# Kernel optimization log

Hardware: AMD Instinct MI355X
Metric: run time of the kernel (lower is better)

The kernel has to match this reference:

```python
import jax, jax.numpy as jnp
import numpy as np

B, S, H, E, K = 8, 4096, 1024, 256, 64
NEG = -1e30  # finite stand-in for -inf to keep grads NaN-free


def setup_inputs() -> dict:
    key = jax.random.key(0)
    ks = jax.random.split(key, 8)
    Hq = H // 4
    sc = 0.02
    return {
        "hidden_states": jax.random.normal(ks[0], (B, S, H), dtype=jnp.float32),
        "attention_mask": jnp.ones((B, S), dtype=jnp.int32),
        "block_boundaries": jnp.sort(jax.random.randint(ks[1], (B, K), 0, S), axis=-1),
        "tok_w1": jax.random.normal(ks[2], (H, Hq), dtype=jnp.float32) * sc,
        "tok_b1": jnp.zeros((Hq,), dtype=jnp.float32),
        "tok_w2": jax.random.normal(ks[3], (Hq, 1), dtype=jnp.float32) * sc,
        "tok_b2": jnp.zeros((1,), dtype=jnp.float32),
        "blk_w1": jax.random.normal(ks[4], (H, Hq), dtype=jnp.float32) * sc,
        "blk_b1": jnp.zeros((Hq,), dtype=jnp.float32),
        "blk_w2": jax.random.normal(ks[5], (Hq, 1), dtype=jnp.float32) * sc,
        "blk_b2": jnp.zeros((1,), dtype=jnp.float32),
        "out_w": jax.random.normal(ks[6], (H, E), dtype=jnp.float32) * sc,
        "out_b": jnp.zeros((E,), dtype=jnp.float32),
    }


def _attn_scores(x, w1, b1, w2, b2):
    # Linear -> Tanh -> Linear(.,1), squeeze last dim
    return (jnp.tanh(x @ w1 + b1) @ w2 + b2)[..., 0]


def reference(hidden_states, attention_mask, block_boundaries,
              tok_w1, tok_b1, tok_w2, tok_b2,
              blk_w1, blk_b1, blk_w2, blk_b2,
              out_w, out_b):
    Bz, Sz, Hz = hidden_states.shape
    Kz = block_boundaries.shape[1]
    pos = jnp.arange(Sz)
    # token -> block id: last boundary <= pos (tokens before first boundary get -1)
    block_id = jax.vmap(lambda bnd: jnp.searchsorted(bnd, pos, side='right') - 1)(block_boundaries)  # [B,S]
    member = block_id[:, :, None] == jnp.arange(Kz)[None, None, :]      # [B,S,K]
    valid = (attention_mask == 1) & (block_id >= 0)                     # [B,S]
    m_full = member & valid[:, :, None]                                 # [B,S,K]

    # stage 1: per-block masked softmax over tokens
    tok_scores = _attn_scores(hidden_states, tok_w1, tok_b1, tok_w2, tok_b2)  # [B,S]
    s = jnp.where(m_full, tok_scores[:, :, None], NEG)
    mx = jnp.max(s, axis=1, keepdims=True)                              # [B,1,K]
    e = jnp.where(m_full, jnp.exp(tok_scores[:, :, None] - mx), 0.0)
    denom = jnp.sum(e, axis=1, keepdims=True)                           # [B,1,K]
    w = jnp.where(denom > 0, e / jnp.maximum(denom, 1e-30), 0.0)
    block_embed = jnp.einsum('bsk,bsd->bkd', w, hidden_states)          # [B,K,H]
    block_valid = denom[:, 0, :] > 0                                    # [B,K] (empty blocks dropped)

    # stage 2: softmax over (non-empty) blocks
    blk_scores = _attn_scores(block_embed, blk_w1, blk_b1, blk_w2, blk_b2)    # [B,K]
    blk_scores = jnp.where(block_valid, blk_scores, NEG)
    bw = jax.nn.softmax(blk_scores, axis=-1)
    func = jnp.einsum('bk,bkd->bd', bw, block_embed)                    # [B,H]

    out = func @ out_w + out_b                                          # [B,E]
    return out / jnp.maximum(jnp.linalg.norm(out, axis=-1, keepdims=True), 1e-12)
```

## Files before the change

kernel.cpp:

```cpp
#include <hip/hip_runtime.h>
#include <math.h>
#include <limits.h>

#define BB 8
#define SS 4096
#define HH 1024
#define EE 256
#define KK 64
#define HQ 256
#define NEGF -1e30f

typedef short bf16x8 __attribute__((ext_vector_type(8)));
typedef float f32x4  __attribute__((ext_vector_type(4)));

__device__ inline short f2bf(float x) {
    unsigned u = __float_as_uint(x);
    unsigned r = (u + 0x7fffu + ((u >> 16) & 1u)) >> 16;
    return (short)r;
}

__device__ inline unsigned pk2bf(float lo, float hi) {
    unsigned a = __float_as_uint(lo) + 0x8000u;
    unsigned b = __float_as_uint(hi) + 0x8000u;
    return (a >> 16) | (b & 0xffff0000u);
}

__global__ __launch_bounds__(256) void convert_both_kernel(
    const float* __restrict__ tok_w1, const float* __restrict__ blk_w1,
    short* __restrict__ w1s_tok, short* __restrict__ w1s_blk)
{
    const int kb = blockIdx.x & 31, which = blockIdx.x >> 5;
    const float* src = which ? blk_w1 : tok_w1;
    short* dst = which ? w1s_blk : w1s_tok;
    const int n = threadIdx.x;
    for (int kk = 0; kk < 32; kk++)
        dst[kb * 8192 + n * 32 + kk] = f2bf(src[(kb * 32 + kk) * HQ + n]);
}

__global__ __launch_bounds__(256, 4) void mfma_score4_kernel(
    const float* __restrict__ X, const short* __restrict__ w1s,
    const float* __restrict__ b1, const float* __restrict__ w2,
    const float* __restrict__ b2, float* __restrict__ out)
{
    __shared__ __attribute__((aligned(16))) short As[2][4][1024];
    __shared__ float part[4][32];

    const int t = threadIdx.x;
    const int wv = t >> 6, lane = t & 63, lo = lane & 15, q = lane >> 4;
    const long row0 = (long)blockIdx.x * 32;

    f32x4 acc[2][4];
#pragma unroll
    for (int i = 0; i < 2; i++)
#pragma unroll
        for (int j = 0; j < 4; j++) acc[i][j] = (f32x4){0.f, 0.f, 0.f, 0.f};

    const int c = t >> 1, half = t & 1;
    const int srow = ((c >> 6) << 4) + (c & 15);
    const int skofs = ((c >> 4) & 3) * 8 + half * 4;
    const float* xs = X + (row0 + srow) * HH + skofs;
    const int dofs = c * 8 + half * 4;
    const short* wp = w1s + (wv * 64 + lo) * 32 + q * 8;

    float4 sv[4];
    bf16x8 bC[4], bN[4];

#pragma unroll
    for (int j = 0; j < 4; j++) sv[j] = *(const float4*)(xs + j * 32);
#pragma unroll
    for (int j = 0; j < 4; j++) {
        unsigned u0 = pk2bf(sv[j].x, sv[j].y), u1 = pk2bf(sv[j].z, sv[j].w);
        unsigned* d = (unsigned*)&As[0][j][dofs];
        d[0] = u0; d[1] = u1;
    }
#pragma unroll
    for (int j = 0; j < 4; j++) sv[j] = *(const float4*)(xs + (4 + j) * 32);
#pragma unroll
    for (int ct = 0; ct < 4; ct++) bC[ct] = *(const bf16x8*)(wp + ct * 512);
    asm volatile("s_waitcnt lgkmcnt(0)" ::: "memory");
    __builtin_amdgcn_sched_barrier(0);
    __builtin_amdgcn_s_barrier();
    __builtin_amdgcn_sched_barrier(0);

#define KSTEP(J, BUSE, BPRE, KBN)                                              \
    {                                                                          \
        _Pragma("unroll")                                                      \
        for (int ct = 0; ct < 4; ct++)                                         \
            BPRE[ct] = *(const bf16x8*)(wp + (KBN) * 8192 + ct * 512);         \
        bf16x8 af0 = *(const bf16x8*)&As[cur][J][(q * 16 + lo) * 8];           \
        bf16x8 af1 = *(const bf16x8*)&As[cur][J][(64 + q * 16 + lo) * 8];      \
        _Pragma("unroll")                                                      \
        for (int ct = 0; ct < 4; ct++) {                                       \
            acc[0][ct] = __builtin_amdgcn_mfma_f32_16x16x32_bf16(              \
                af0, BUSE[ct], acc[0][ct], 0, 0, 0);                           \
            acc[1][ct] = __builtin_amdgcn_mfma_f32_16x16x32_bf16(              \
                af1, BUSE[ct], acc[1][ct], 0, 0, 0);                           \
        }                                                                      \
    }

    for (int ci = 0; ci < 8; ci++) {
        const int cur = ci & 1;
        const int kb0 = ci * 4;
        KSTEP(0, bC, bN, kb0 + 1)
        KSTEP(1, bN, bC, kb0 + 2)
        KSTEP(2, bC, bN, kb0 + 3)
        const int kbn3 = (kb0 + 4 < 32) ? kb0 + 4 : 31;
        KSTEP(3, bN, bC, kbn3)
        if (ci < 7) {
#pragma unroll
            for (int j = 0; j < 4; j++) {
                unsigned u0 = pk2bf(sv[j].x, sv[j].y), u1 = pk2bf(sv[j].z, sv[j].w);
                unsigned* d = (unsigned*)&As[cur ^ 1][j][dofs];
                d[0] = u0; d[1] = u1;
            }
            const int cn = (ci + 2 < 8) ? ci + 2 : 7;
#pragma unroll
            for (int j = 0; j < 4; j++)
                sv[j] = *(const float4*)(xs + (cn * 4 + j) * 32);
        }
        asm volatile("s_waitcnt lgkmcnt(0)" ::: "memory");
        __builtin_amdgcn_sched_barrier(0);
        __builtin_amdgcn_s_barrier();
        __builtin_amdgcn_sched_barrier(0);
    }
#undef KSTEP

    float rowpart[2][4];
#pragma unroll
    for (int rt = 0; rt < 2; rt++)
#pragma unroll
        for (int r = 0; r < 4; r++) rowpart[rt][r] = 0.f;
#pragma unroll
    for (int ct = 0; ct < 4; ct++) {
        const int cc = wv * 64 + ct * 16 + lo;
        const float b1c = b1[cc], w2c = w2[cc];
#pragma unroll
        for (int rt = 0; rt < 2; rt++)
#pragma unroll
            for (int r = 0; r < 4; r++)
                rowpart[rt][r] += tanhf(acc[rt][ct][r] + b1c) * w2c;
    }
#pragma unroll
    for (int rt = 0; rt < 2; rt++)
#pragma unroll
        for (int r = 0; r < 4; r++) {
            float v = rowpart[rt][r];
            v += __shfl_down(v, 8, 64);
            v += __shfl_down(v, 4, 64);
            v += __shfl_down(v, 2, 64);
            v += __shfl_down(v, 1, 64);
            rowpart[rt][r] = v;
        }
    if (lo == 0)
#pragma unroll
        for (int rt = 0; rt < 2; rt++)
#pragma unroll
            for (int r = 0; r < 4; r++)
                part[wv][rt * 16 + q * 4 + r] = rowpart[rt][r];
    __syncthreads();
    if (t < 32)
        out[row0 + t] = part[0][t] + part[1][t] + part[2][t] + part[3][t] + b2[0];
}

__global__ __launch_bounds__(256) void block_stats_kernel(
    const float* __restrict__ scores, const int* __restrict__ mask,
    const int* __restrict__ bnd, float* __restrict__ bden,
    float* __restrict__ wtok)
{
    const int b = blockIdx.x >> 6, k = blockIdx.x & 63;
    const int start = bnd[b * KK + k];
    const int end = (k == KK - 1) ? SS : bnd[b * KK + k + 1];
    const int tid = threadIdx.x;
    __shared__ float r[4];
    __shared__ float mshared, dshared;

    if (k == 0)
        for (int s = tid; s < start; s += 256) wtok[b * SS + s] = 0.f;

    float m = NEGF;
    for (int s = start + tid; s < end; s += 256)
        if (mask[b * SS + s] == 1) m = fmaxf(m, scores[b * SS + s]);
    for (int off = 32; off > 0; off >>= 1) m = fmaxf(m, __shfl_down(m, off, 64));
    if ((tid & 63) == 0) r[tid >> 6] = m;
    __syncthreads();
    if (tid == 0) mshared = fmaxf(fmaxf(r[0], r[1]), fmaxf(r[2], r[3]));
    __syncthreads();
    m = mshared;

    float d = 0.f;
    for (int s = start + tid; s < end; s += 256)
        if (mask[b * SS + s] == 1) d += expf(scores[b * SS + s] - m);
    for (int off = 32; off > 0; off >>= 1) d += __shfl_down(d, off, 64);
    __syncthreads();
    if ((tid & 63) == 0) r[tid >> 6] = d;
    __syncthreads();
    if (tid == 0) {
        float den = r[0] + r[1] + r[2] + r[3];
        bden[blockIdx.x] = den;
        dshared = (den > 0.f) ? 1.f / fmaxf(den, 1e-30f) : 0.f;
    }
    __syncthreads();
    const float inv = dshared;
    for (int s = start + tid; s < end; s += 256)
        wtok[b * SS + s] = (mask[b * SS + s] == 1) ? expf(scores[b * SS + s] - m) * inv : 0.f;
}

__global__ __launch_bounds__(256) void block_embed_direct_kernel(
    const float* __restrict__ hidden, const float* __restrict__ wtok,
    const int* __restrict__ bnd, float* __restrict__ embed)
{
    const int bk = blockIdx.x >> 2;
    const int hq = blockIdx.x & 3;
    const int b = bk >> 6, k = bk & 63;
    const int start = bnd[bk];
    const int end = (k == KK - 1) ? SS : bnd[bk + 1];
    const int n = end - start;
    const int t = threadIdx.x;
    const int col = hq * 256 + t;

    const float* hp = hidden + ((long)b * SS + start) * HH + col;
    const float* wp = wtok + b * SS + start;

    float acc = 0.f;
    int s = 0;
    for (; s + 4 <= n; s += 4) {
        const float w0 = wp[s],     w1 = wp[s + 1];
        const float w2 = wp[s + 2], w3 = wp[s + 3];
        const float h0 = hp[(long)s * HH],      h1 = hp[(long)(s + 1) * HH];
        const float h2 = hp[(long)(s + 2) * HH], h3 = hp[(long)(s + 3) * HH];
        acc = fmaf(w0, h0, acc);
        acc = fmaf(w1, h1, acc);
        acc = fmaf(w2, h2, acc);
        acc = fmaf(w3, h3, acc);
    }
    for (; s < n; s++)
        acc = fmaf(wp[s], hp[(long)s * HH], acc);

    embed[(long)bk * HH + col] = acc;
}

__global__ __launch_bounds__(256) void finalize_ab_kernel(
    const float* __restrict__ embed, const float* __restrict__ bscores,
    const float* __restrict__ bden, const float* __restrict__ out_w,
    float* __restrict__ osum)
{
    const int b = blockIdx.x >> 5;
    const int hc = (blockIdx.x >> 2) & 7;
    const int hq = blockIdx.x & 3;
    const int t = threadIdx.x;
    __shared__ float bw[KK];
    __shared__ float fpart[8][32];
    __shared__ float fsh[32];

    if (t < KK) {
        float s = (bden[b * KK + t] > 0.f) ? bscores[b * KK + t] : NEGF;
        float m = s;
        for (int off = 32; off > 0; off >>= 1) m = fmaxf(m, __shfl_xor(m, off, 64));
        float e = expf(s - m);
        float d = e;
        for (int off = 32; off > 0; off >>= 1) d += __shfl_xor(d, off, 64);
        bw[t] = e / d;
    }
    __syncthreads();

    const int hbase = hc * 128 + hq * 32;
    {
        const int hh = t & 31, kh = t >> 5;
        const float* ep = embed + ((long)b * KK + kh * 8) * HH + hbase + hh;
        float f = 0.f;
#pragma unroll
        for (int k2 = 0; k2 < 8; k2++)
            f = fmaf(bw[kh * 8 + k2], ep[(long)k2 * HH], f);
        fpart[kh][hh] = f;
    }
    __syncthreads();
    if (t < 32) {
        float f = 0.f;
#pragma unroll
        for (int g = 0; g < 8; g++) f += fpart[g][t];
        fsh[t] = f;
    }
    __syncthreads();

    float acc = 0.f;
    const float* wpp = out_w + (long)hbase * EE + t;
#pragma unroll
    for (int h = 0; h < 32; h++)
        acc = fmaf(fsh[h], wpp[(long)h * EE], acc);
    osum[(long)(b * 32 + hc * 4 + hq) * EE + t] = acc;
}

__global__ __launch_bounds__(256) void finalize_c_kernel(
    const float* __restrict__ osum, const float* __restrict__ out_b,
    float* __restrict__ outp)
{
    const int b = blockIdx.x, t = threadIdx.x;
    __shared__ float r4[4];
    float o = out_b[t];
#pragma unroll
    for (int hc = 0; hc < 32; hc++)
        o += osum[(long)(b * 32 + hc) * EE + t];
    float sq = o * o;
    for (int off = 32; off > 0; off >>= 1) sq += __shfl_down(sq, off, 64);
    if ((t & 63) == 0) r4[t >> 6] = sq;
    __syncthreads();
    const float nrm = sqrtf(r4[0] + r4[1] + r4[2] + r4[3]);
    outp[b * EE + t] = o / fmaxf(nrm, 1e-12f);
}

extern "C" void kernel_launch(void* const* d_in, const int* in_sizes, int n_in,
                              void* d_out, int out_size, void* d_ws, size_t ws_size,
                              hipStream_t stream) {
    const float* hidden  = (const float*)d_in[0];
    const int*   mask    = (const int*)  d_in[1];
    const int*   bnd     = (const int*)  d_in[2];
    const float* tok_w1  = (const float*)d_in[3];
    const float* tok_b1  = (const float*)d_in[4];
    const float* tok_w2  = (const float*)d_in[5];
    const float* tok_b2  = (const float*)d_in[6];
    const float* blk_w1  = (const float*)d_in[7];
    const float* blk_b1  = (const float*)d_in[8];
    const float* blk_w2  = (const float*)d_in[9];
    const float* blk_b2  = (const float*)d_in[10];
    const float* out_w   = (const float*)d_in[11];
    const float* out_b   = (const float*)d_in[12];

    float* ws      = (float*)d_ws;
    float* wtok    = ws;
    float* embed   = ws + 32768;
    float* scores  = ws + 557056;
    float* bden    = ws + 589824;
    float* bscores = ws + 590336;
    float* osum    = ws + 590848;
    short* w1s_tok = (short*)(ws + 656384);
    short* w1s_blk = w1s_tok + 262144;

    convert_both_kernel<<<64, 256, 0, stream>>>(tok_w1, blk_w1, w1s_tok, w1s_blk);
    mfma_score4_kernel<<<BB * SS / 32, 256, 0, stream>>>(
        hidden, w1s_tok, tok_b1, tok_w2, tok_b2, scores);
    block_stats_kernel<<<BB * KK, 256, 0, stream>>>(
        scores, mask, bnd, bden, wtok);
    block_embed_direct_kernel<<<BB * KK * 4, 256, 0, stream>>>(
        hidden, wtok, bnd, embed);
    mfma_score4_kernel<<<BB * KK / 32, 256, 0, stream>>>(
        embed, w1s_blk, blk_b1, blk_w2, blk_b2, bscores);
    finalize_ab_kernel<<<BB * 32, 256, 0, stream>>>(
        embed, bscores, bden, out_w, osum);
    finalize_c_kernel<<<BB, 256, 0, stream>>>(osum, out_b, (float*)d_out);
}
```

Baseline: 299.3 us.

## Fuse token scoring with block-embedding accumulation via atomics, dropping max subtraction

After: 311.5 us. +4.1%, slower.

```diff
diff --git a/kernel.cpp b/kernel.cpp
--- a/kernel.cpp
+++ b/kernel.cpp
@@ -37,17 +37,38 @@
         dst[kb * 8192 + n * 32 + kk] = f2bf(src[(kb * 32 + kk) * HQ + n]);
 }
 
-__global__ __launch_bounds__(256, 4) void mfma_score4_kernel(
+__global__ __launch_bounds__(256) void zero_ws_kernel(
+    float* __restrict__ embed, float* __restrict__ den)
+{
+    const int t = threadIdx.x;
+    if (blockIdx.x < 512) {
+        float* e = embed + (long)blockIdx.x * HH + t;
+        e[0] = 0.f; e[256] = 0.f; e[512] = 0.f; e[768] = 0.f;
+    } else {
+        den[t] = 0.f; den[t + 256] = 0.f;
+    }
+}
+
+__global__ __launch_bounds__(256, 4) void mfma_score_embed_kernel(
     const float* __restrict__ X, const short* __restrict__ w1s,
     const float* __restrict__ b1, const float* __restrict__ w2,
-    const float* __restrict__ b2, float* __restrict__ out)
+    const float* __restrict__ b2, const int* __restrict__ mask,
+    const int* __restrict__ bnd, float* __restrict__ den,
+    float* __restrict__ embed)
 {
     __shared__ __attribute__((aligned(16))) short As[2][4][1024];
     __shared__ float part[4][32];
+    __shared__ float wrow[32];
+    __shared__ int kid[32];
+    __shared__ int bsh[KK];
 
     const int t = threadIdx.x;
     const int wv = t >> 6, lane = t & 63, lo = lane & 15, q = lane >> 4;
     const long row0 = (long)blockIdx.x * 32;
+    const int bb = (int)(row0 >> 12);
+    const int s0 = (int)(row0 & (SS - 1));
+
+    if (t < KK) bsh[t] = bnd[bb * KK + t];
 
     f32x4 acc[2][4];
 #pragma unroll
@@ -158,85 +179,189 @@
             for (int r = 0; r < 4; r++)
                 part[wv][rt * 16 + q * 4 + r] = rowpart[rt][r];
     __syncthreads();
+
+    if (t < 32) {
+        const float sc = part[0][t] + part[1][t] + part[2][t] + part[3][t] + b2[0];
+        const int s = s0 + t;
+        int k = -1;
+#pragma unroll
+        for (int i = 0; i < KK; i++) k = (bsh[i] <= s) ? i : k;
+        kid[t] = k;
+        const bool valid = (k >= 0) && (mask[bb * SS + s] == 1);
+        const float w = valid ? expf(sc) : 0.f;
+        wrow[t] = w;
+        if (w > 0.f) atomicAdd(&den[bb * KK + k], w);
+    }
+    __syncthreads();
+
+    {
+        const float* hb = X + row0 * HH + t;
+        float* eb = embed + (long)bb * KK * HH + t;
+        float r0 = 0.f, r1 = 0.f, r2 = 0.f, r3 = 0.f;
+        int prevk = -1;
+        bool any = false;
+        for (int r = 0; r < 32; r++) {
+            const int k = kid[r];
+            if (k != prevk) {
+                if (any) {
+                    float* e = eb + (long)prevk * HH;
+                    atomicAdd(e, r0); atomicAdd(e + 256, r1);
+                    atomicAdd(e + 512, r2); atomicAdd(e + 768, r3);
+                    r0 = r1 = r2 = r3 = 0.f; any = false;
+                }
+                prevk = k;
+            }
+            const float w = wrow[r];
+            if (w != 0.f) {
+                const float* hr = hb + (long)r * HH;
+                r0 = fmaf(w, hr[0], r0);
+                r1 = fmaf(w, hr[256], r1);
+                r2 = fmaf(w, hr[512], r2);
+                r3 = fmaf(w, hr[768], r3);
+                any = true;
+            }
+        }
+        if (any) {
+            float* e = eb + (long)prevk * HH;
+            atomicAdd(e, r0); atomicAdd(e + 256, r1);
+            atomicAdd(e + 512, r2); atomicAdd(e + 768, r3);
+        }
+    }
+}
+
+__global__ __launch_bounds__(256) void embed_norm_kernel(
+    float* __restrict__ embed, const float* __restrict__ den)
+{
+    const int bk = blockIdx.x, t = threadIdx.x;
+    const float d = den[bk];
+    const float inv = (d > 0.f) ? 1.f / d : 0.f;
+    float* e = embed + (long)bk * HH + t;
+    e[0] *= inv; e[256] *= inv; e[512] *= inv; e[768] *= inv;
+}
+
+__global__ __launch_bounds__(256, 4) void mfma_score4_kernel(
+    const float* __restrict__ X, const short* __restrict__ w1s,
+    const float* __restrict__ b1, const float* __restrict__ w2,
+    const float* __restrict__ b2, float* __restrict__ out)
+{
+    __shared__ __attribute__((aligned(16))) short As[2][4][1024];
+    __shared__ float part[4][32];
+
+    const int t = threadIdx.x;
+    const int wv = t >> 6, lane = t & 63, lo = lane & 15, q = lane >> 4;
+    const long row0 = (long)blockIdx.x * 32;
+
+    f32x4 acc[2][4];
+#pragma unroll
+    for (int i = 0; i < 2; i++)
+#pragma unroll
+        for (int j = 0; j < 4; j++) acc[i][j] = (f32x4){0.f, 0.f, 0.f, 0.f};
+
+    const int c = t >> 1, half = t & 1;
+    const int srow = ((c >> 6) << 4) + (c & 15);
+    const int skofs = ((c >> 4) & 3) * 8 + half * 4;
+    const float* xs = X + (row0 + srow) * HH + skofs;
+    const int dofs = c * 8 + half * 4;
+    const short* wp = w1s + (wv * 64 + lo) * 32 + q * 8;
+
+    float4 sv[4];
+    bf16x8 bC[4], bN[4];
+
+#pragma unroll
+    for (int j = 0; j < 4; j++) sv[j] = *(const float4*)(xs + j * 32);
+#pragma unroll
+    for (int j = 0; j < 4; j++) {
+        unsigned u0 = pk2bf(sv[j].x, sv[j].y), u1 = pk2bf(sv[j].z, sv[j].w);
+        unsigned* d = (unsigned*)&As[0][j][dofs];
+        d[0] = u0; d[1] = u1;
+    }
+#pragma unroll
+    for (int j = 0; j < 4; j++) sv[j] = *(const float4*)(xs + (4 + j) * 32);
+#pragma unroll
+    for (int ct = 0; ct < 4; ct++) bC[ct] = *(const bf16x8*)(wp + ct * 512);
+    asm volatile("s_waitcnt lgkmcnt(0)" ::: "memory");
+    __builtin_amdgcn_sched_barrier(0);
+    __builtin_amdgcn_s_barrier();
+    __builtin_amdgcn_sched_barrier(0);
+
+#define KSTEP(J, BUSE, BPRE, KBN)                                              \
+    {                                                                          \
+        _Pragma("unroll")                                                      \
+        for (int ct = 0; ct < 4; ct++)                                         \
+            BPRE[ct] = *(const bf16x8*)(wp + (KBN) * 8192 + ct * 512);         \
+        bf16x8 af0 = *(const bf16x8*)&As[cur][J][(q * 16 + lo) * 8];           \
+        bf16x8 af1 = *(const bf16x8*)&As[cur][J][(64 + q * 16 + lo) * 8];      \
+        _Pragma("unroll")                                                      \
+        for (int ct = 0; ct < 4; ct++) {                                       \
+            acc[0][ct] = __builtin_amdgcn_mfma_f32_16x16x32_bf16(              \
+                af0, BUSE[ct], acc[0][ct], 0, 0, 0);                           \
+            acc[1][ct] = __builtin_amdgcn_mfma_f32_16x16x32_bf16(              \
+                af1, BUSE[ct], acc[1][ct], 0, 0, 0);                           \
+        }                                                                      \
+    }
+
+    for (int ci = 0; ci < 8; ci++) {
+        const int cur = ci & 1;
+        const int kb0 = ci * 4;
+        KSTEP(0, bC, bN, kb0 + 1)
+        KSTEP(1, bN, bC, kb0 + 2)
+        KSTEP(2, bC, bN, kb0 + 3)
+        const int kbn3 = (kb0 + 4 < 32) ? kb0 + 4 : 31;
+        KSTEP(3, bN, bC, kbn3)
+        if (ci < 7) {
+#pragma unroll
+            for (int j = 0; j < 4; j++) {
+                unsigned u0 = pk2bf(sv[j].x, sv[j].y), u1 = pk2bf(sv[j].z, sv[j].w);
+                unsigned* d = (unsigned*)&As[cur ^ 1][j][dofs];
+                d[0] = u0; d[1] = u1;
+            }
+            const int cn = (ci + 2 < 8) ? ci + 2 : 7;
+#pragma unroll
+            for (int j = 0; j < 4; j++)
+                sv[j] = *(const float4*)(xs + (cn * 4 + j) * 32);
+        }
+        asm volatile("s_waitcnt lgkmcnt(0)" ::: "memory");
+        __builtin_amdgcn_sched_barrier(0);
+        __builtin_amdgcn_s_barrier();
+        __builtin_amdgcn_sched_barrier(0);
+    }
+#undef KSTEP
+
+    float rowpart[2][4];
+#pragma unroll
+    for (int rt = 0; rt < 2; rt++)
+#pragma unroll
+        for (int r = 0; r < 4; r++) rowpart[rt][r] = 0.f;
+#pragma unroll
+    for (int ct = 0; ct < 4; ct++) {
+        const int cc = wv * 64 + ct * 16 + lo;
+        const float b1c = b1[cc], w2c = w2[cc];
+#pragma unroll
+        for (int rt = 0; rt < 2; rt++)
+#pragma unroll
+            for (int r = 0; r < 4; r++)
+                rowpart[rt][r] += tanhf(acc[rt][ct][r] + b1c) * w2c;
+    }
+#pragma unroll
+    for (int rt = 0; rt < 2; rt++)
+#pragma unroll
+        for (int r = 0; r < 4; r++) {
+            float v = rowpart[rt][r];
+            v += __shfl_down(v, 8, 64);
+            v += __shfl_down(v, 4, 64);
+            v += __shfl_down(v, 2, 64);
+            v += __shfl_down(v, 1, 64);
+            rowpart[rt][r] = v;
+        }
+    if (lo == 0)
+#pragma unroll
+        for (int rt = 0; rt < 2; rt++)
+#pragma unroll
+            for (int r = 0; r < 4; r++)
+                part[wv][rt * 16 + q * 4 + r] = rowpart[rt][r];
+    __syncthreads();
     if (t < 32)
         out[row0 + t] = part[0][t] + part[1][t] + part[2][t] + part[3][t] + b2[0];
-}
-
-__global__ __launch_bounds__(256) void block_stats_kernel(
-    const float* __restrict__ scores, const int* __restrict__ mask,
-    const int* __restrict__ bnd, float* __restrict__ bden,
-    float* __restrict__ wtok)
-{
-    const int b = blockIdx.x >> 6, k = blockIdx.x & 63;
-    const int start = bnd[b * KK + k];
-    const int end = (k == KK - 1) ? SS : bnd[b * KK + k + 1];
-    const int tid = threadIdx.x;
-    __shared__ float r[4];
-    __shared__ float mshared, dshared;
-
-    if (k == 0)
-        for (int s = tid; s < start; s += 256) wtok[b * SS + s] = 0.f;
-
-    float m = NEGF;
-    for (int s = start + tid; s < end; s += 256)
-        if (mask[b * SS + s] == 1) m = fmaxf(m, scores[b * SS + s]);
-    for (int off = 32; off > 0; off >>= 1) m = fmaxf(m, __shfl_down(m, off, 64));
-    if ((tid & 63) == 0) r[tid >> 6] = m;
-    __syncthreads();
-    if (tid == 0) mshared = fmaxf(fmaxf(r[0], r[1]), fmaxf(r[2], r[3]));
-    __syncthreads();
-    m = mshared;
-
-    float d = 0.f;
-    for (int s = start + tid; s < end; s += 256)
-        if (mask[b * SS + s] == 1) d += expf(scores[b * SS + s] - m);
-    for (int off = 32; off > 0; off >>= 1) d += __shfl_down(d, off, 64);
-    __syncthreads();
-    if ((tid & 63) == 0) r[tid >> 6] = d;
-    __syncthreads();
-    if (tid == 0) {
-        float den = r[0] + r[1] + r[2] + r[3];
-        bden[blockIdx.x] = den;
-        dshared = (den > 0.f) ? 1.f / fmaxf(den, 1e-30f) : 0.f;
-    }
-    __syncthreads();
-    const float inv = dshared;
-    for (int s = start + tid; s < end; s += 256)
-        wtok[b * SS + s] = (mask[b * SS + s] == 1) ? expf(scores[b * SS + s] - m) * inv : 0.f;
-}
-
-__global__ __launch_bounds__(256) void block_embed_direct_kernel(
-    const float* __restrict__ hidden, const float* __restrict__ wtok,
-    const int* __restrict__ bnd, float* __restrict__ embed)
-{
-    const int bk = blockIdx.x >> 2;
-    const int hq = blockIdx.x & 3;
-    const int b = bk >> 6, k = bk & 63;
-    const int start = bnd[bk];
-    const int end = (k == KK - 1) ? SS : bnd[bk + 1];
-    const int n = end - start;
-    const int t = threadIdx.x;
-    const int col = hq * 256 + t;
-
-    const float* hp = hidden + ((long)b * SS + start) * HH + col;
-    const float* wp = wtok + b * SS + start;
-
-    float acc = 0.f;
-    int s = 0;
-    for (; s + 4 <= n; s += 4) {
-        const float w0 = wp[s],     w1 = wp[s + 1];
-        const float w2 = wp[s + 2], w3 = wp[s + 3];
-        const float h0 = hp[(long)s * HH],      h1 = hp[(long)(s + 1) * HH];
-        const float h2 = hp[(long)(s + 2) * HH], h3 = hp[(long)(s + 3) * HH];
-        acc = fmaf(w0, h0, acc);
-        acc = fmaf(w1, h1, acc);
-        acc = fmaf(w2, h2, acc);
-        acc = fmaf(w3, h3, acc);
-    }
-    for (; s < n; s++)
-        acc = fmaf(wp[s], hp[(long)s * HH], acc);
-
-    embed[(long)bk * HH + col] = acc;
 }
 
 __global__ __launch_bounds__(256) void finalize_ab_kernel(
@@ -326,9 +451,7 @@
     const float* out_b   = (const float*)d_in[12];
 
     float* ws      = (float*)d_ws;
-    float* wtok    = ws;
     float* embed   = ws + 32768;
-    float* scores  = ws + 557056;
     float* bden    = ws + 589824;
     float* bscores = ws + 590336;
     float* osum    = ws + 590848;
@@ -336,12 +459,10 @@
     short* w1s_blk = w1s_tok + 262144;
 
     convert_both_kernel<<<64, 256, 0, stream>>>(tok_w1, blk_w1, w1s_tok, w1s_blk);
-    mfma_score4_kernel<<<BB * SS / 32, 256, 0, stream>>>(
-        hidden, w1s_tok, tok_b1, tok_w2, tok_b2, scores);
-    block_stats_kernel<<<BB * KK, 256, 0, stream>>>(
-        scores, mask, bnd, bden, wtok);
-    block_embed_direct_kernel<<<BB * KK * 4, 256, 0, stream>>>(
-        hidden, wtok, bnd, embed);
+    zero_ws_kernel<<<513, 256, 0, stream>>>(embed, bden);
+    mfma_score_embed_kernel<<<BB * SS / 32, 256, 0, stream>>>(
+        hidden, w1s_tok, tok_b1, tok_w2, tok_b2, mask, bnd, bden, embed);
+    embed_norm_kernel<<<BB * KK, 256, 0, stream>>>(embed, bden);
     mfma_score4_kernel<<<BB * KK / 32, 256, 0, stream>>>(
         embed, w1s_blk, blk_b1, blk_w2, blk_b2, bscores);
     finalize_ab_kernel<<<BB * 32, 256, 0, stream>>>(
```
